# Kernel tuning notes

Hardware: AMD Instinct MI355X
Metric: run time of the kernel (lower is better)

Reference implementation:

```python
import jax, jax.numpy as jnp
import numpy as np

MAX_W, MIN_W = 120, 24


def setup_inputs() -> dict:
    key = jax.random.key(0)
    ks = jax.random.split(key, 11)
    B, S, D, H = 2, 2048, 1024, 16
    hd = D // H
    s = 1.0 / float(np.sqrt(D))
    return {
        "x": jax.random.normal(ks[0], (B, S, D), jnp.float32),
        "alpha": jnp.float32(0.1),
        "Wq": jax.random.normal(ks[1], (D, D), jnp.float32) * s,
        "bq": jnp.zeros((D,), jnp.float32),
        "Wk": jax.random.normal(ks[2], (D, D), jnp.float32) * s,
        "bk": jnp.zeros((D,), jnp.float32),
        "Wv": jax.random.normal(ks[3], (D, D), jnp.float32) * s,
        "bv": jnp.zeros((D,), jnp.float32),
        "W_o": jax.random.normal(ks[4], (H, hd, hd), jnp.float32),
        "Wfc": jax.random.normal(ks[5], (D, D), jnp.float32) * s,
        "bfc": jnp.zeros((D,), jnp.float32),
    }


def reference(x, alpha, Wq, bq, Wk, bk, Wv, bv, W_o, Wfc, bfc):
    B, S, D = x.shape
    H, hd, _ = W_o.shape
    # --- dynamic window size (step==0 path of the module) ---
    fluct = jnp.abs(x[:, -1] - x[:, -2])            # [B, D]
    a = jax.nn.sigmoid(alpha)
    ewma_prev = fluct[0, 0]                          # step==0: ewma_prev = fluct_step_value
    signal = a * fluct.mean() + (1.0 - a) * ewma_prev
    scale = jax.nn.sigmoid(signal)
    w = jnp.floor(MIN_W + (MAX_W - MIN_W) * scale).astype(jnp.int32)  # int() truncation
    half = w // 2
    # --- projections ---
    q = (x @ Wq + bq).reshape(B, S, H, hd).transpose(0, 2, 1, 3)  # [B,H,S,hd]
    k = (x @ Wk + bk).reshape(B, S, H, hd).transpose(0, 2, 1, 3)
    v = (x @ Wv + bv).reshape(B, S, H, hd).transpose(0, 2, 1, 3)
    inv_sqrt = 1.0 / float(np.sqrt(hd))
    scores = jnp.einsum('bhqd,bhkd->bhqk', q, k) * inv_sqrt       # [B,H,S,S]
    # banded window mask: allowed iff i - w//2 <= j <= i + w//2
    idx = jnp.arange(S)
    band = jnp.abs(idx[:, None] - idx[None, :]) <= half            # [S,S]
    scores = jnp.where(band[None, None], scores, -1e30)
    attn = jax.nn.softmax(scores, axis=-1)
    out = jnp.einsum('bhqk,bhkd->bhqd', attn, v)                   # [B,H,S,hd]
    out = jnp.einsum('bhqd,hdk->bhqk', out, W_o)                   # per-head output matmul
    out = out.transpose(0, 2, 1, 3).reshape(B, S, D)
    return out @ Wfc + bfc
```

## Files before the change

### kernel.cpp

```cpp
#include <hip/hip_runtime.h>
#include <hip/hip_bf16.h>
#include <stdint.h>
#include <stddef.h>

#define S_LEN 2048
#define DMODEL 1024
#define NHEAD 16
#define HDIM 64
#define BATCH 2
#define MROWS (BATCH * S_LEN)
#define QKV_LD 3072

typedef unsigned short u16;
typedef __attribute__((ext_vector_type(8))) short bf16x8;
typedef __attribute__((ext_vector_type(4))) float f32x4;

__device__ inline u16 f32_to_bf16(float f) {
  union { float f; unsigned int u; } v; v.f = f;
  unsigned int u = v.u;
  unsigned int r = (u + 0x7fffu + ((u >> 16) & 1u)) >> 16;
  return (u16)r;
}

__device__ inline void gload16(const u16* g, u16* l) {
  __builtin_amdgcn_global_load_lds(
      (const __attribute__((address_space(1))) unsigned int*)g,
      (__attribute__((address_space(3))) unsigned int*)l, 16, 0, 0);
}

__global__ __launch_bounds__(256) void prep(const float* __restrict__ x, u16* __restrict__ xb,
                                            const float* __restrict__ alpha, int* __restrict__ halfw,
                                            const float* __restrict__ Wq, const float* __restrict__ Wk,
                                            const float* __restrict__ Wv, u16* __restrict__ Wt) {
  __shared__ float lds[32 * 33];
  const int bid = blockIdx.x, tid = threadIdx.x;

  if (bid < 2048) {
    size_t i = ((size_t)bid * 256 + tid) * 8;
    float4 v0 = *(const float4*)(x + i);
    float4 v1 = *(const float4*)(x + i + 4);
    bf16x8 r;
    r[0] = (short)f32_to_bf16(v0.x); r[1] = (short)f32_to_bf16(v0.y);
    r[2] = (short)f32_to_bf16(v0.z); r[3] = (short)f32_to_bf16(v0.w);
    r[4] = (short)f32_to_bf16(v1.x); r[5] = (short)f32_to_bf16(v1.y);
    r[6] = (short)f32_to_bf16(v1.z); r[7] = (short)f32_to_bf16(v1.w);
    *(bf16x8*)(xb + i) = r;
  } else if (bid == 2048) {
    float s = 0.f;
    for (int i = tid; i < BATCH * DMODEL; i += 256) {
      int b = i >> 10, d = i & 1023;
      size_t base = (size_t)b * S_LEN * DMODEL + d;
      float f1 = x[base + (size_t)(S_LEN - 1) * DMODEL];
      float f0 = x[base + (size_t)(S_LEN - 2) * DMODEL];
      s += fabsf(f1 - f0);
    }
#pragma unroll
    for (int m = 32; m >= 1; m >>= 1) s += __shfl_xor(s, m, 64);
    if ((tid & 63) == 0) lds[tid >> 6] = s;
    __syncthreads();
    if (tid == 0) {
      float total = lds[0] + lds[1] + lds[2] + lds[3];
      float mean = total / (float)(BATCH * DMODEL);
      float e1 = x[(size_t)(S_LEN - 1) * DMODEL];
      float e0 = x[(size_t)(S_LEN - 2) * DMODEL];
      float ew = fabsf(e1 - e0);
      float a = 1.f / (1.f + expf(-alpha[0]));
      float sig = a * mean + (1.f - a) * ew;
      float scale = 1.f / (1.f + expf(-sig));
      int wv = (int)floorf(24.f + 96.f * scale);
      *halfw = wv >> 1;
    }
  } else {
    float (*tile)[33] = (float (*)[33])lds;
    const int r = bid - 2049;
    const int z = r >> 10, rem = r & 1023;
    const int k0 = (rem >> 5) * 32, n0 = (rem & 31) * 32;
    const float* W = z == 0 ? Wq : (z == 1 ? Wk : Wv);
    const int tx = tid & 31, ty = tid >> 5;
#pragma unroll
    for (int i = 0; i < 4; ++i)
      tile[ty + i * 8][tx] = W[(size_t)(k0 + ty + i * 8) * DMODEL + n0 + tx];
    __syncthreads();
    u16* o = Wt + (size_t)z * DMODEL * DMODEL;
#pragma unroll
    for (int i = 0; i < 4; ++i)
      o[(size_t)(n0 + ty + i * 8) * DMODEL + k0 + tx] = f32_to_bf16(tile[tx][ty + i * 8]);
  }
}

__global__ __launch_bounds__(128) void build_wc(const float* __restrict__ W_o,
                                                const float* __restrict__ Wfc,
                                                u16* __restrict__ Wc_t) {
  __shared__ float lds[64 * 128];
  int nb = blockIdx.x, h = blockIdx.y, tx = threadIdx.x;
  int n0 = nb * 128;
#pragma unroll
  for (int c = 0; c < 64; ++c)
    lds[c * 128 + tx] = Wfc[(size_t)(h * 64 + c) * DMODEL + n0 + tx];
  __syncthreads();
  float acc[64];
#pragma unroll
  for (int d = 0; d < 64; ++d) acc[d] = 0.f;
  for (int c = 0; c < 64; ++c) {
    float wv = lds[c * 128 + tx];
#pragma unroll
    for (int d = 0; d < 64; ++d)
      acc[d] += W_o[(size_t)(h * 64 + d) * 64 + c] * wv;
  }
  u16 tmp[64];
#pragma unroll
  for (int d = 0; d < 64; ++d) tmp[d] = f32_to_bf16(acc[d]);
  u16* dst = Wc_t + (size_t)(n0 + tx) * DMODEL + h * 64;
#pragma unroll
  for (int q = 0; q < 8; ++q)
    *(bf16x8*)(dst + q * 8) = *(bf16x8*)(tmp + q * 8);
}

#define G1_ASZ (256 * 64)
#define G1_BSZ (192 * 64)
__global__ __launch_bounds__(512, 2) void gemm_qkv(
    const u16* __restrict__ A, const u16* __restrict__ Bt,
    const float* __restrict__ bq, const float* __restrict__ bk,
    const float* __restrict__ bv, u16* __restrict__ out) {
  __shared__ __align__(16) u16 smem[2][G1_ASZ + G1_BSZ];

  const int tid = threadIdx.x;
  const int l = tid & 63, w = tid >> 6;
  const int wr = w >> 2, wc = w & 3;
  const int lrow = l & 15, lk = l >> 4;

  const int xcd = blockIdx.x & 7;
  const int idx = blockIdx.x >> 3;
  const int bm = idx & 15;
  const int bn = xcd * 2 + (idx >> 4);
  const int rowA0 = bm * 256;
  const int colB0 = bn * 192;

  f32x4 acc[8][3] = {};

  auto stage = [&](int buf, int kt) {
    u16* As = smem[buf];
    u16* Bs = smem[buf] + G1_ASZ;
#pragma unroll
    for (int i = 0; i < 4; ++i) {
      int c = i * 512 + tid;
      int row = c >> 3, u = c & 7;
      const u16* g = A + (size_t)(rowA0 + row) * DMODEL + kt + ((u ^ (row & 7)) << 3);
      gload16(g, As + c * 8);
    }
#pragma unroll
    for (int i = 0; i < 3; ++i) {
      int c = i * 512 + tid;
      int row = c >> 3, u = c & 7;
      const u16* g = Bt + (size_t)(colB0 + row) * DMODEL + kt + ((u ^ (row & 7)) << 3);
      gload16(g, Bs + c * 8);
    }
  };

  stage(0, 0);

  int buf = 0;
#pragma unroll 1
  for (int t = 0; t < 16; ++t) {
    __builtin_amdgcn_s_barrier();
    if (t < 15) {
      stage(buf ^ 1, (t + 1) * 64);
      asm volatile("s_waitcnt vmcnt(7)" ::: "memory");
    } else {
      asm volatile("s_waitcnt vmcnt(0)" ::: "memory");
    }
    __builtin_amdgcn_s_barrier();
    asm volatile("" ::: "memory");

    const u16* As = smem[buf];
    const u16* Bs = smem[buf] + G1_ASZ;
    __builtin_amdgcn_s_setprio(1);
#pragma unroll
    for (int kk = 0; kk < 2; ++kk) {
      const int swz = ((((kk << 2) + lk) ^ (lrow & 7)) << 3);
      bf16x8 bg[3], af[8];
#pragma unroll
      for (int n = 0; n < 3; ++n)
        bg[n] = *(const bf16x8*)(Bs + (wc * 48 + n * 16 + lrow) * 64 + swz);
#pragma unroll
      for (int m = 0; m < 8; ++m)
        af[m] = *(const bf16x8*)(As + (wr * 128 + m * 16 + lrow) * 64 + swz);
#pragma unroll
      for (int m = 0; m < 8; ++m)
#pragma unroll
        for (int n = 0; n < 3; ++n)
          acc[m][n] = __builtin_amdgcn_mfma_f32_16x16x32_bf16(af[m], bg[n], acc[m][n], 0, 0, 0);
    }
    __builtin_amdgcn_s_setprio(0);
    buf ^= 1;
  }

#pragma unroll
  for (int n = 0; n < 3; ++n) {
    int c = colB0 + wc * 48 + n * 16 + lrow;
    float bias = (c < 1024) ? bq[c] : ((c < 2048) ? bk[c - 1024] : bv[c - 2048]);
    float mult = (c < 1024) ? 0.125f : 1.0f;
#pragma unroll
    for (int m = 0; m < 8; ++m) {
      int r0 = rowA0 + wr * 128 + m * 16 + lk * 4;
#pragma unroll
      for (int j = 0; j < 4; ++j)
        out[(size_t)(r0 + j) * QKV_LD + c] = f32_to_bf16((acc[m][n][j] + bias) * mult);
    }
  }
}

__global__ __launch_bounds__(256) void gemm_fc(const u16* __restrict__ A,
                                               const u16* __restrict__ Bt,
                                               const float* __restrict__ bias,
                                               float* __restrict__ out) {
  __shared__ __align__(16) u16 smem[2][256 * 64];

  const int tid = threadIdx.x;
  const int l = tid & 63, w = tid >> 6;
  const int wr = w >> 1, wc = w & 1;
  const int lrow = l & 15, lk = l >> 4;

  const int bn = blockIdx.x & 7;
  const int bm = blockIdx.x >> 3;
  const int rowA0 = bm * 128, colB0 = bn * 128;

  f32x4 acc[4][4] = {};

  auto stage = [&](int buf, int kt) {
    u16* As = smem[buf];
    u16* Bs = smem[buf] + 128 * 64;
#pragma unroll
    for (int i = 0; i < 4; ++i) {
      int c = i * 256 + tid;
      int row = c >> 3, u = c & 7;
      const u16* g = A + (size_t)(rowA0 + row) * DMODEL + kt + ((u ^ (row & 7)) << 3);
      gload16(g, As + c * 8);
    }
#pragma unroll
    for (int i = 0; i < 4; ++i) {
      int c = i * 256 + tid;
      int row = c >> 3, u = c & 7;
      const u16* g = Bt + (size_t)(colB0 + row) * DMODEL + kt + ((u ^ (row & 7)) << 3);
      gload16(g, Bs + c * 8);
    }
  };

  stage(0, 0);

  int buf = 0;
#pragma unroll 1
  for (int t = 0; t < 16; ++t) {
    __builtin_amdgcn_s_barrier();
    if (t < 15) {
      stage(buf ^ 1, (t + 1) * 64);
      asm volatile("s_waitcnt vmcnt(8)" ::: "memory");
    } else {
      asm volatile("s_waitcnt vmcnt(0)" ::: "memory");
    }
    __builtin_amdgcn_s_barrier();
    asm volatile("" ::: "memory");

    const u16* As = smem[buf];
    const u16* Bs = smem[buf] + 128 * 64;
    __builtin_amdgcn_s_setprio(1);
#pragma unroll
    for (int kk = 0; kk < 2; ++kk) {
      const int swz = ((((kk << 2) + lk) ^ (lrow & 7)) << 3);
      bf16x8 af[4], bg[4];
#pragma unroll
      for (int m = 0; m < 4; ++m)
        af[m] = *(const bf16x8*)(As + (wr * 64 + m * 16 + lrow) * 64 + swz);
#pragma unroll
      for (int n = 0; n < 4; ++n)
        bg[n] = *(const bf16x8*)(Bs + (wc * 64 + n * 16 + lrow) * 64 + swz);
#pragma unroll
      for (int m = 0; m < 4; ++m)
#pragma unroll
        for (int n = 0; n < 4; ++n)
          acc[m][n] = __builtin_amdgcn_mfma_f32_16x16x32_bf16(af[m], bg[n], acc[m][n], 0, 0, 0);
    }
    __builtin_amdgcn_s_setprio(0);
    buf ^= 1;
  }

#pragma unroll
  for (int n = 0; n < 4; ++n) {
    int c = colB0 + wc * 64 + n * 16 + lrow;
    float bv = bias[c];
#pragma unroll
    for (int m = 0; m < 4; ++m) {
      int r0 = rowA0 + wr * 64 + m * 16 + lk * 4;
#pragma unroll
      for (int j = 0; j < 4; ++j)
        out[(size_t)(r0 + j) * DMODEL + c] = acc[m][n][j] + bv;
    }
  }
}

__global__ __launch_bounds__(256) void attn_win(const u16* __restrict__ qkv,
                                                u16* __restrict__ ao,
                                                const int* __restrict__ halfptr) {
  __shared__ __align__(16) u16 KP[12800];
  __shared__ __align__(16) u16 Vt[64 * 200];
  const int tid = threadIdx.x, l = tid & 63, w = tid >> 6;
  const int lrow = l & 15, lk = l >> 4;
  const int q0 = blockIdx.x * 64, k0 = q0 - 64;
  const int h = blockIdx.y, b = blockIdx.z;
  const int halfw = *halfptr;
  const int f_lo = (64 - halfw) >> 4;
  const int f_hi = (127 + halfw) >> 4;

  const u16* qb = qkv;
  const u16* kb = qkv + 1024;
  const u16* vb = qkv + 2048;

#pragma unroll
  for (int i = 0; i < 6; ++i) {
    int c = i * 256 + tid;
    int row = c >> 3, u = c & 7;
    const u16* g = kb + (ptrdiff_t)((b * S_LEN + k0 + row) * QKV_LD + h * 64 + ((u ^ (row & 7)) << 3));
    gload16(g, KP + c * 8);
  }
  const int qrow = q0 + w * 16 + lrow;
  bf16x8 qf[2];
#pragma unroll
  for (int kk = 0; kk < 2; ++kk)
    qf[kk] = *(const bf16x8*)(qb + (ptrdiff_t)((b * S_LEN + qrow) * QKV_LD + h * 64 + kk * 32 + lk * 8));
  bf16x8 vreg[6];
#pragma unroll
  for (int i = 0; i < 6; ++i) {
    int c = i * 256 + tid;
    int row = c % 192, ch = c / 192;
    vreg[i] = *(const bf16x8*)(vb + (ptrdiff_t)((b * S_LEN + k0 + row) * QKV_LD + h * 64 + ch * 8));
  }

  asm volatile("s_waitcnt vmcnt(0)" ::: "memory");
  __syncthreads();

  f32x4 sc[12];
#pragma unroll
  for (int f = 0; f < 12; ++f) sc[f] = (f32x4){0.f, 0.f, 0.f, 0.f};
#pragma unroll
  for (int kk = 0; kk < 2; ++kk) {
#pragma unroll
    for (int f = 0; f < 12; ++f) {
      if (f >= f_lo && f <= f_hi) {
        bf16x8 kf = *(const bf16x8*)(KP + (f * 16 + lrow) * 64 + ((((kk << 2) + lk) ^ (lrow & 7)) << 3));
        sc[f] = __builtin_amdgcn_mfma_f32_16x16x32_bf16(qf[kk], kf, sc[f], 0, 0, 0);
      }
    }
  }

#pragma unroll
  for (int i = 0; i < 6; ++i) {
    int c = i * 256 + tid;
    int row = c % 192, ch = c / 192;
#pragma unroll
    for (int e = 0; e < 8; ++e)
      Vt[(ch * 8 + e) * 200 + row] = (u16)vreg[i][e];
  }

  float rmax[4] = {-3e38f, -3e38f, -3e38f, -3e38f};
  const int qbase = q0 + w * 16 + lk * 4;
#pragma unroll
  for (int f = 0; f < 12; ++f) {
    if (f < f_lo || f > f_hi) continue;
    int kj = k0 + f * 16 + lrow;
    bool kok = (kj >= 0) && (kj < S_LEN);
#pragma unroll
    for (int j = 0; j < 4; ++j) {
      int qi = qbase + j;
      float v = sc[f][j];
      int dd = qi - kj;
      int ad = dd < 0 ? -dd : dd;
      v = (kok && ad <= halfw) ? v : -1e30f;
      sc[f][j] = v;
      rmax[j] = fmaxf(rmax[j], v);
    }
  }
#pragma unroll
  for (int j = 0; j < 4; ++j) {
    rmax[j] = fmaxf(rmax[j], __shfl_xor(rmax[j], 1, 16));
    rmax[j] = fmaxf(rmax[j], __shfl_xor(rmax[j], 2, 16));
    rmax[j] = fmaxf(rmax[j], __shfl_xor(rmax[j], 4, 16));
    rmax[j] = fmaxf(rmax[j], __shfl_xor(rmax[j], 8, 16));
  }
  float rsum[4] = {0.f, 0.f, 0.f, 0.f};
#pragma unroll
  for (int f = 0; f < 12; ++f) {
    if (f < f_lo || f > f_hi) { sc[f] = (f32x4){0.f, 0.f, 0.f, 0.f}; continue; }
#pragma unroll
    for (int j = 0; j < 4; ++j) {
      float e = __expf(sc[f][j] - rmax[j]);
      sc[f][j] = e;
      rsum[j] += e;
    }
  }
#pragma unroll
  for (int j = 0; j < 4; ++j) {
    rsum[j] += __shfl_xor(rsum[j], 1, 16);
    rsum[j] += __shfl_xor(rsum[j], 2, 16);
    rsum[j] += __shfl_xor(rsum[j], 4, 16);
    rsum[j] += __shfl_xor(rsum[j], 8, 16);
  }
  float rinv[4];
#pragma unroll
  for (int j = 0; j < 4; ++j) rinv[j] = 1.0f / rsum[j];

  __syncthreads();

  u16* Ps = KP;
#pragma unroll
  for (int f = 0; f < 12; ++f)
#pragma unroll
    for (int j = 0; j < 4; ++j) {
      int prow = w * 16 + lk * 4 + j;
      Ps[prow * 200 + f * 16 + lrow] = f32_to_bf16(sc[f][j] * rinv[j]);
    }
  __syncthreads();

  f32x4 o[4] = {};
#pragma unroll
  for (int jt = 0; jt < 6; ++jt) {
    bf16x8 pa = *(const bf16x8*)(Ps + (w * 16 + lrow) * 200 + jt * 32 + lk * 8);
#pragma unroll
    for (int n = 0; n < 4; ++n) {
      bf16x8 vf = *(const bf16x8*)(Vt + (n * 16 + lrow) * 200 + jt * 32 + lk * 8);
      o[n] = __builtin_amdgcn_mfma_f32_16x16x32_bf16(pa, vf, o[n], 0, 0, 0);
    }
  }
#pragma unroll
  for (int n = 0; n < 4; ++n)
#pragma unroll
    for (int j = 0; j < 4; ++j) {
      int qi = q0 + w * 16 + lk * 4 + j;
      int d = n * 16 + lrow;
      ao[(size_t)(b * S_LEN + qi) * DMODEL + h * 64 + d] = f32_to_bf16(o[n][j]);
    }
}

extern "C" void kernel_launch(void* const* d_in, const int* in_sizes, int n_in,
                              void* d_out, int out_size, void* d_ws, size_t ws_size,
                              hipStream_t stream) {
  (void)in_sizes; (void)n_in; (void)out_size; (void)ws_size;
  const float* x     = (const float*)d_in[0];
  const float* alpha = (const float*)d_in[1];
  const float* Wq    = (const float*)d_in[2];
  const float* bq    = (const float*)d_in[3];
  const float* Wk    = (const float*)d_in[4];
  const float* bk    = (const float*)d_in[5];
  const float* Wv    = (const float*)d_in[6];
  const float* bv    = (const float*)d_in[7];
  const float* W_o   = (const float*)d_in[8];
  const float* Wfc   = (const float*)d_in[9];
  const float* bfc   = (const float*)d_in[10];

  char* ws = (char*)d_ws;
  int* halfw  = (int*)ws;
  u16* xb     = (u16*)(ws + 256);
  u16* Wqkv_t = xb + (size_t)MROWS * DMODEL;
  u16* qkv    = Wqkv_t + (size_t)3 * DMODEL * DMODEL;
  u16* ao     = qkv + (size_t)MROWS * QKV_LD;
  u16* Wc_t   = ao + (size_t)MROWS * DMODEL;

  hipLaunchKernelGGL(prep, dim3(5121), dim3(256), 0, stream,
                     x, xb, alpha, halfw, Wq, Wk, Wv, Wqkv_t);
  hipLaunchKernelGGL(build_wc, dim3(8, 16), dim3(128), 0, stream, W_o, Wfc, Wc_t);
  hipLaunchKernelGGL(gemm_qkv, dim3(256), dim3(512), 0, stream,
                     xb, Wqkv_t, bq, bk, bv, qkv);
  hipLaunchKernelGGL(attn_win, dim3(S_LEN / 64, NHEAD, BATCH), dim3(256), 0, stream,
                     qkv, ao, halfw);
  hipLaunchKernelGGL(gemm_fc, dim3(256), dim3(256), 0, stream,
                     ao, Wc_t, bfc, (float*)d_out);
}
```

Measured before the change: 103.0 us.

## Write V transposed from QKV GEMM and async-load it in attention

The QKV GEMM epilogue now writes V in a transposed [B, D, S] layout (packed 4-wide stores) instead of interleaving it into the QKV buffer. The attention kernel loads V straight into LDS with global_load_lds, which removes the register-held V tile and the scalar LDS transpose scatter. It also uses partial waitcnt with raw barriers so the V load can overlap the QK^T stage. The FC GEMM block index is remapped so each XCD gets contiguous row blocks. The risk is less coalesced V stores in the GEMM epilogue and extra clamped out-of-range V loads at the sequence edges.

Measured after the change: 104.9 us. About the same (+1.8%).

```diff
diff --git a/kernel.cpp b/kernel.cpp
--- a/kernel.cpp
+++ b/kernel.cpp
@@ -9,10 +9,11 @@
 #define HDIM 64
 #define BATCH 2
 #define MROWS (BATCH * S_LEN)
-#define QKV_LD 3072
+#define QK_LD 2048
 
 typedef unsigned short u16;
 typedef __attribute__((ext_vector_type(8))) short bf16x8;
+typedef __attribute__((ext_vector_type(4))) short bf16x4;
 typedef __attribute__((ext_vector_type(4))) float f32x4;
 
 __device__ inline u16 f32_to_bf16(float f) {
@@ -121,7 +122,7 @@
 __global__ __launch_bounds__(512, 2) void gemm_qkv(
     const u16* __restrict__ A, const u16* __restrict__ Bt,
     const float* __restrict__ bq, const float* __restrict__ bk,
-    const float* __restrict__ bv, u16* __restrict__ out) {
+    const float* __restrict__ bv, u16* __restrict__ out, u16* __restrict__ vt) {
   __shared__ __align__(16) u16 smem[2][G1_ASZ + G1_BSZ];
 
   const int tid = threadIdx.x;
@@ -198,14 +199,28 @@
 #pragma unroll
   for (int n = 0; n < 3; ++n) {
     int c = colB0 + wc * 48 + n * 16 + lrow;
-    float bias = (c < 1024) ? bq[c] : ((c < 2048) ? bk[c - 1024] : bv[c - 2048]);
-    float mult = (c < 1024) ? 0.125f : 1.0f;
-#pragma unroll
-    for (int m = 0; m < 8; ++m) {
-      int r0 = rowA0 + wr * 128 + m * 16 + lk * 4;
-#pragma unroll
-      for (int j = 0; j < 4; ++j)
-        out[(size_t)(r0 + j) * QKV_LD + c] = f32_to_bf16((acc[m][n][j] + bias) * mult);
+    if (c < 2048) {
+      float bias = (c < 1024) ? bq[c] : bk[c - 1024];
+      float mult = (c < 1024) ? 0.125f : 1.0f;
+#pragma unroll
+      for (int m = 0; m < 8; ++m) {
+        int r0 = rowA0 + wr * 128 + m * 16 + lk * 4;
+#pragma unroll
+        for (int j = 0; j < 4; ++j)
+          out[(size_t)(r0 + j) * QK_LD + c] = f32_to_bf16((acc[m][n][j] + bias) * mult);
+      }
+    } else {
+      const int dfull = c - 2048;
+      const float bias = bv[dfull];
+#pragma unroll
+      for (int m = 0; m < 8; ++m) {
+        int r0 = rowA0 + wr * 128 + m * 16 + lk * 4;
+        int bb = r0 >> 11, s = r0 & 2047;
+        bf16x4 p;
+#pragma unroll
+        for (int j = 0; j < 4; ++j) p[j] = (short)f32_to_bf16(acc[m][n][j] + bias);
+        *(bf16x4*)(vt + ((size_t)bb << 21) + (size_t)dfull * 2048 + s) = p;
+      }
     }
   }
 }
@@ -221,8 +236,10 @@
   const int wr = w >> 1, wc = w & 1;
   const int lrow = l & 15, lk = l >> 4;
 
-  const int bn = blockIdx.x & 7;
-  const int bm = blockIdx.x >> 3;
+  const int xcd = blockIdx.x & 7;
+  const int idx = blockIdx.x >> 3;
+  const int bn = idx >> 2;
+  const int bm = xcd * 4 + (idx & 3);
   const int rowA0 = bm * 128, colB0 = bn * 128;
 
   f32x4 acc[4][4] = {};
@@ -299,10 +316,11 @@
 }
 
 __global__ __launch_bounds__(256) void attn_win(const u16* __restrict__ qkv,
+                                                const u16* __restrict__ vt,
                                                 u16* __restrict__ ao,
                                                 const int* __restrict__ halfptr) {
   __shared__ __align__(16) u16 KP[12800];
-  __shared__ __align__(16) u16 Vt[64 * 200];
+  __shared__ __align__(16) u16 Vs[12800];
   const int tid = threadIdx.x, l = tid & 63, w = tid >> 6;
   const int lrow = l & 15, lk = l >> 4;
   const int q0 = blockIdx.x * 64, k0 = q0 - 64;
@@ -313,30 +331,42 @@
 
   const u16* qb = qkv;
   const u16* kb = qkv + 1024;
-  const u16* vb = qkv + 2048;
 
 #pragma unroll
   for (int i = 0; i < 6; ++i) {
     int c = i * 256 + tid;
     int row = c >> 3, u = c & 7;
-    const u16* g = kb + (ptrdiff_t)((b * S_LEN + k0 + row) * QKV_LD + h * 64 + ((u ^ (row & 7)) << 3));
+    const u16* g = kb + (ptrdiff_t)((b * S_LEN + k0 + row) * QK_LD + h * 64 + ((u ^ (row & 7)) << 3));
     gload16(g, KP + c * 8);
   }
   const int qrow = q0 + w * 16 + lrow;
   bf16x8 qf[2];
 #pragma unroll
   for (int kk = 0; kk < 2; ++kk)
-    qf[kk] = *(const bf16x8*)(qb + (ptrdiff_t)((b * S_LEN + qrow) * QKV_LD + h * 64 + kk * 32 + lk * 8));
-  bf16x8 vreg[6];
+    qf[kk] = *(const bf16x8*)(qb + (ptrdiff_t)((b * S_LEN + qrow) * QK_LD + h * 64 + kk * 32 + lk * 8));
 #pragma unroll
   for (int i = 0; i < 6; ++i) {
-    int c = i * 256 + tid;
-    int row = c % 192, ch = c / 192;
-    vreg[i] = *(const bf16x8*)(vb + (ptrdiff_t)((b * S_LEN + k0 + row) * QKV_LD + h * 64 + ch * 8));
-  }
-
-  asm volatile("s_waitcnt vmcnt(0)" ::: "memory");
-  __syncthreads();
+    int o = i * 256 + tid;
+    int d = o / 25, ch = o - d * 25;
+    int kc = k0 + ch * 8;
+    kc = kc < 0 ? 0 : (kc > 2040 ? 2040 : kc);
+    const u16* g = vt + ((size_t)b << 21) + (size_t)(h * 64 + d) * 2048 + kc;
+    gload16(g, Vs + o * 8);
+  }
+  {
+    int o = 1536 + tid;
+    if (o < 1600) {
+      int d = o / 25, ch = o - d * 25;
+      int kc = k0 + ch * 8;
+      kc = kc < 0 ? 0 : (kc > 2040 ? 2040 : kc);
+      const u16* g = vt + ((size_t)b << 21) + (size_t)(h * 64 + d) * 2048 + kc;
+      gload16(g, Vs + o * 8);
+    }
+  }
+
+  asm volatile("s_waitcnt vmcnt(6)" ::: "memory");
+  __builtin_amdgcn_s_barrier();
+  asm volatile("" ::: "memory");
 
   f32x4 sc[12];
 #pragma unroll
@@ -350,15 +380,6 @@
         sc[f] = __builtin_amdgcn_mfma_f32_16x16x32_bf16(qf[kk], kf, sc[f], 0, 0, 0);
       }
     }
-  }
-
-#pragma unroll
-  for (int i = 0; i < 6; ++i) {
-    int c = i * 256 + tid;
-    int row = c % 192, ch = c / 192;
-#pragma unroll
-    for (int e = 0; e < 8; ++e)
-      Vt[(ch * 8 + e) * 200 + row] = (u16)vreg[i][e];
   }
 
   float rmax[4] = {-3e38f, -3e38f, -3e38f, -3e38f};
@@ -408,7 +429,8 @@
 #pragma unroll
   for (int j = 0; j < 4; ++j) rinv[j] = 1.0f / rsum[j];
 
-  __syncthreads();
+  __builtin_amdgcn_s_barrier();
+  asm volatile("" ::: "memory");
 
   u16* Ps = KP;
 #pragma unroll
@@ -418,7 +440,9 @@
       int prow = w * 16 + lk * 4 + j;
       Ps[prow * 200 + f * 16 + lrow] = f32_to_bf16(sc[f][j] * rinv[j]);
     }
-  __syncthreads();
+  asm volatile("s_waitcnt lgkmcnt(0) vmcnt(0)" ::: "memory");
+  __builtin_amdgcn_s_barrier();
+  asm volatile("" ::: "memory");
 
   f32x4 o[4] = {};
 #pragma unroll
@@ -426,7 +450,7 @@
     bf16x8 pa = *(const bf16x8*)(Ps + (w * 16 + lrow) * 200 + jt * 32 + lk * 8);
 #pragma unroll
     for (int n = 0; n < 4; ++n) {
-      bf16x8 vf = *(const bf16x8*)(Vt + (n * 16 + lrow) * 200 + jt * 32 + lk * 8);
+      bf16x8 vf = *(const bf16x8*)(Vs + (n * 16 + lrow) * 200 + jt * 32 + lk * 8);
       o[n] = __builtin_amdgcn_mfma_f32_16x16x32_bf16(pa, vf, o[n], 0, 0, 0);
     }
   }
@@ -461,16 +485,17 @@
   u16* xb     = (u16*)(ws + 256);
   u16* Wqkv_t = xb + (size_t)MROWS * DMODEL;
   u16* qkv    = Wqkv_t + (size_t)3 * DMODEL * DMODEL;
-  u16* ao     = qkv + (size_t)MROWS * QKV_LD;
+  u16* vt     = qkv + (size_t)MROWS * QK_LD;
+  u16* ao     = vt + (size_t)BATCH * DMODEL * S_LEN;
   u16* Wc_t   = ao + (size_t)MROWS * DMODEL;
 
   hipLaunchKernelGGL(prep, dim3(5121), dim3(256), 0, stream,
                      x, xb, alpha, halfw, Wq, Wk, Wv, Wqkv_t);
   hipLaunchKernelGGL(build_wc, dim3(8, 16), dim3(128), 0, stream, W_o, Wfc, Wc_t);
   hipLaunchKernelGGL(gemm_qkv, dim3(256), dim3(512), 0, stream,
-                     xb, Wqkv_t, bq, bk, bv, qkv);
+                     xb, Wqkv_t, bq, bk, bv, qkv, vt);
   hipLaunchKernelGGL(attn_win, dim3(S_LEN / 64, NHEAD, BATCH), dim3(256), 0, stream,
-                     qkv, ao, halfw);
+                     qkv, vt, ao, halfw);
   hipLaunchKernelGGL(gemm_fc, dim3(256), dim3(256), 0, stream,
                      ao, Wc_t, bfc, (float*)d_out);
 }
```
